# Kernel optimization log

Measured on AMD Instinct MI355X. Metric: run time of the kernel, lower is better.

## Reference

```python
import jax, jax.numpy as jnp
import numpy as np

NUM_NODES = 100000
NUM_REL = 500
D = 400          # entity_out_dim[0] * nheads_GAT[0] = 200 * 2
C = 50           # conv_out_channels
B = 16384        # batch of triples


def setup_inputs() -> dict:
    key = jax.random.key(0)
    k = jax.random.split(key, 7)
    entity_emb = jax.random.normal(k[0], (NUM_NODES, D), jnp.float32)
    relation_emb = jax.random.normal(k[1], (NUM_REL, D), jnp.float32)
    # Conv2d(1, C, (1, 3)) weight: [C, 1, 1, 3]; xavier-ish scale
    conv_w = jax.random.normal(k[2], (C, 1, 1, 3), jnp.float32) * 0.5
    conv_b = jnp.zeros((C,), jnp.float32)
    # Linear(D*C, 1)
    fc_w = jax.random.normal(k[3], (1, D * C), jnp.float32) * 0.01
    fc_b = jnp.zeros((1,), jnp.float32)
    heads = jax.random.randint(k[4], (B,), 0, NUM_NODES)
    rels = jax.random.randint(k[5], (B,), 0, NUM_REL)
    tails = jax.random.randint(k[6], (B,), 0, NUM_NODES)
    batch_inputs = jnp.stack([heads, rels, tails], axis=1)  # [B, 3]
    return {
        "entity_emb": entity_emb,
        "relation_emb": relation_emb,
        "conv_w": conv_w,
        "conv_b": conv_b,
        "fc_w": fc_w,
        "fc_b": fc_b,
        "batch_inputs": batch_inputs,
    }


def reference(entity_emb, relation_emb, conv_w, conv_b, fc_w, fc_b, batch_inputs):
    # Gather (h, r, t) rows: irregular access into large tables
    h = entity_emb[batch_inputs[:, 0]]    # [B, D]
    r = relation_emb[batch_inputs[:, 1]]  # [B, D]
    t = entity_emb[batch_inputs[:, 2]]    # [B, D]
    # torch: cat -> [B, 3, D], transpose -> [B, D, 3], unsqueeze -> [B, 1, D, 3]
    x = jnp.stack([h, r, t], axis=-1)     # [B, D, 3]
    # Conv2d(1, C, (1, 3)): kernel spans full width -> per-channel dot over 3
    w = conv_w[:, 0, 0, :]                # [C, 3]
    out = jnp.einsum("bdk,ck->bcd", x, w) + conv_b[None, :, None]  # [B, C, D]
    out = jax.nn.relu(out)                # dropout is identity in eval mode
    # squeeze(-1).view(B, -1): channel-major flatten -> [B, C*D]
    flat = out.reshape(out.shape[0], -1)
    return flat @ fc_w.T + fc_b           # [B, 1]
```

## Files before the change

### kernel.cpp

```cpp
#include <hip/hip_runtime.h>


typedef _Float16 h2 __attribute__((ext_vector_type(2)));
typedef _Float16 h8 __attribute__((ext_vector_type(8)));

constexpr int D    = 400;
constexpr int CP   = 25;
constexpr int DPAD = 404;

static __device__ __forceinline__ float dot2acc(h2 a, h2 b, float c) {
#if __has_builtin(__builtin_amdgcn_fdot2)
    return __builtin_amdgcn_fdot2(a, b, c, false);
#else
    h2 p = a * b; return c + (float)p[0] + (float)p[1];
#endif
}
static __device__ __forceinline__ h2 dup(float v) {
    _Float16 x = (_Float16)v; h2 r; r[0] = x; r[1] = x; return r;
}

__global__ __attribute__((amdgpu_flat_work_group_size(512, 512), amdgpu_waves_per_eu(2, 4)))
void grcnet_pk16g(
    const float* __restrict__ entity_emb,
    const float* __restrict__ relation_emb,
    const float* __restrict__ conv_w,
    const float* __restrict__ conv_b,
    const float* __restrict__ fc_w,
    const float* __restrict__ fc_b,
    const int*   __restrict__ batch_inputs,
    float* __restrict__ out,
    int nB)
{
    __shared__ h2    fc_lds[CP + 1][DPAD];
    __shared__ h2    conv_lds[CP + 1][4];
    __shared__ float partials[2][2][4][4];

    const int tid  = threadIdx.x;
    const int lane = tid & 63;
    const int wv   = tid >> 6;
    const int grp  = wv >> 1;
    const int hc   = wv & 1;
    const int bq   = blockIdx.x * 32;
    if (bq >= nB) return;

    const float *p0h, *p0r, *p0t, *p1h, *p1r, *p1t;
    const float *p2h, *p2r, *p2t, *p3h, *p3r, *p3t;

    #define SETPTRS(B0)                                                           \
    {                                                                             \
        const int bbase = __builtin_amdgcn_readfirstlane((B0) + 4 * grp);         \
        const int* bi = batch_inputs + 3 * bbase;                                 \
        p0h = entity_emb   + (size_t)bi[0]  * D + lane;                           \
        p0r = relation_emb + (size_t)bi[1]  * D + lane;                           \
        p0t = entity_emb   + (size_t)bi[2]  * D + lane;                           \
        p1h = entity_emb   + (size_t)bi[3]  * D + lane;                           \
        p1r = relation_emb + (size_t)bi[4]  * D + lane;                           \
        p1t = entity_emb   + (size_t)bi[5]  * D + lane;                           \
        p2h = entity_emb   + (size_t)bi[6]  * D + lane;                           \
        p2r = relation_emb + (size_t)bi[7]  * D + lane;                           \
        p2t = entity_emb   + (size_t)bi[8]  * D + lane;                           \
        p3h = entity_emb   + (size_t)bi[9]  * D + lane;                           \
        p3r = relation_emb + (size_t)bi[10] * D + lane;                           \
        p3t = entity_emb   + (size_t)bi[11] * D + lane;                           \
    }

    #define LOADI(S, IDX)                                                         \
        f##S##_0h = p0h[IDX]; f##S##_0r = p0r[IDX]; f##S##_0t = p0t[IDX];         \
        f##S##_1h = p1h[IDX]; f##S##_1r = p1r[IDX]; f##S##_1t = p1t[IDX];         \
        f##S##_2h = p2h[IDX]; f##S##_2r = p2r[IDX]; f##S##_2t = p2t[IDX];         \
        f##S##_3h = p3h[IDX]; f##S##_3r = p3r[IDX]; f##S##_3t = p3t[IDX];

    float fA_0h, fA_0r, fA_0t, fA_1h, fA_1r, fA_1t;
    float fA_2h, fA_2r, fA_2t, fA_3h, fA_3r, fA_3t;
    float fB_0h, fB_0r, fB_0t, fB_1h, fB_1r, fB_1t;
    float fB_2h, fB_2r, fB_2t, fB_3h, fB_3r, fB_3t;

    SETPTRS(bq)
    LOADI(A, 0)
    LOADI(B, 64)

    for (int k = tid; k < CP * 100; k += 512) {
        const int cp = k / 100;
        const int dq = k - cp * 100;
        const float4 A  = *(const float4*)(fc_w + (2*cp)     * D + 4*dq);
        const float4 Bv = *(const float4*)(fc_w + (2*cp + 1) * D + 4*dq);
        h8 g;
        g[0]=(_Float16)A.x; g[1]=(_Float16)Bv.x;
        g[2]=(_Float16)A.y; g[3]=(_Float16)Bv.y;
        g[4]=(_Float16)A.z; g[5]=(_Float16)Bv.z;
        g[6]=(_Float16)A.w; g[7]=(_Float16)Bv.w;
        *(h8*)&fc_lds[cp][4*dq] = g;
    }
    {
        h2 z; z[0] = (_Float16)0; z[1] = (_Float16)0;
        if (tid < CP * 4) fc_lds[tid >> 2][D + (tid & 3)] = z;
        if (tid >= 64 && tid < 64 + DPAD) fc_lds[CP][tid - 64] = z;
    }
    if (tid < CP + 1) {
        const int src = (tid == CP) ? (CP - 1) : tid;
        const int c0 = 2 * src;
        h2 wa, wb, wc, cb;
        wa[0]=(_Float16)conv_w[3*c0+0]; wa[1]=(_Float16)conv_w[3*c0+3];
        wb[0]=(_Float16)conv_w[3*c0+1]; wb[1]=(_Float16)conv_w[3*c0+4];
        wc[0]=(_Float16)conv_w[3*c0+2]; wc[1]=(_Float16)conv_w[3*c0+5];
        cb[0]=(_Float16)conv_b[c0];     cb[1]=(_Float16)conv_b[c0+1];
        conv_lds[tid][0]=wa; conv_lds[tid][1]=wb;
        conv_lds[tid][2]=wc; conv_lds[tid][3]=cb;
    }
    __syncthreads();

    const int C0 = 13 * hc;
    constexpr int NC = 13;
    h2 cwa[NC], cwb[NC], cwc[NC], ccb[NC];
    #pragma unroll
    for (int j = 0; j < NC; ++j) {
        cwa[j] = conv_lds[C0+j][0]; cwb[j] = conv_lds[C0+j][1];
        cwc[j] = conv_lds[C0+j][2]; ccb[j] = conv_lds[C0+j][3];
    }

    const int  d6 = lane + 384;
    const bool a6 = (d6 < D);
    const int  i6 = a6 ? 384 : -lane;
    const h2* fcb  = &fc_lds[0][0] + C0 * DPAD + lane;
    const h2* fcb6 = &fc_lds[0][0] + C0 * DPAD + (a6 ? d6 : D);

    const h2 zero2 = (h2)(_Float16)0;

    #define COMPUTE(S, FB, FIDX0)                                                 \
    {                                                                             \
        const h2 H0 = dup(f##S##_0h), R0 = dup(f##S##_0r), T0 = dup(f##S##_0t);   \
        const h2 H1 = dup(f##S##_1h), R1 = dup(f##S##_1r), T1 = dup(f##S##_1t);   \
        const h2 H2 = dup(f##S##_2h), R2 = dup(f##S##_2r), T2 = dup(f##S##_2t);   \
        const h2 H3 = dup(f##S##_3h), R3 = dup(f##S##_3r), T3 = dup(f##S##_3t);   \
        _Pragma("unroll")                                                         \
        for (int j = 0; j < NC; ++j) {                                            \
            const h2 f2 = (FB)[(FIDX0) + j * DPAD];               \
            h2 s0 = H0*cwa[j] + (R0*cwb[j] + (T0*cwc[j] + ccb[j]));               \
            h2 s1 = H1*cwa[j] + (R1*cwb[j] + (T1*cwc[j] + ccb[j]));               \
            h2 s2 = H2*cwa[j] + (R2*cwb[j] + (T2*cwc[j] + ccb[j]));               \
            h2 s3 = H3*cwa[j] + (R3*cwb[j] + (T3*cwc[j] + ccb[j]));               \
            s0 = __builtin_elementwise_max(s0, zero2);                            \
            s1 = __builtin_elementwise_max(s1, zero2);                            \
            s2 = __builtin_elementwise_max(s2, zero2);                            \
            s3 = __builtin_elementwise_max(s3, zero2);                            \
            acc0 = dot2acc(s0, f2, acc0);                                         \
            acc1 = dot2acc(s1, f2, acc1);                                         \
            acc2 = dot2acc(s2, f2, acc2);                                         \
            acc3 = dot2acc(s3, f2, acc3);                                         \
        }                                                                         \
    }

    #pragma unroll 1
    for (int g = 0; g < 2; ++g) {
        const int b0 = bq + 16 * g;
        if (b0 >= nB) break;
        if (g) {
            SETPTRS(b0)
            LOADI(A, 0)
            LOADI(B, 64)
        }
        float acc0 = 0.f, acc1 = 0.f, acc2 = 0.f, acc3 = 0.f;

        LOADI(A, 128)
        (void)0;
        acc0 = 0.f; acc1 = 0.f; acc2 = 0.f; acc3 = 0.f;
        if (g) { LOADI(A, 0) LOADI(B, 64) }
        else   { LOADI(A, 0) LOADI(B, 64) }

        COMPUTE(A, fcb, 0*64)   LOADI(A, 128)
        COMPUTE(B, fcb, 1*64)   LOADI(B, 192)
        COMPUTE(A, fcb, 2*64)   LOADI(A, 256)
        COMPUTE(B, fcb, 3*64)   LOADI(B, 320)
        COMPUTE(A, fcb, 4*64)   LOADI(A, i6)
        COMPUTE(B, fcb, 5*64)
        COMPUTE(A, fcb6, 0)

        #pragma unroll
        for (int off = 32; off > 0; off >>= 1) {
            acc0 += __shfl_xor(acc0, off);
            acc1 += __shfl_xor(acc1, off);
            acc2 += __shfl_xor(acc2, off);
            acc3 += __shfl_xor(acc3, off);
        }
        if (lane == 0) {
            partials[g][hc][grp][0] = acc0; partials[g][hc][grp][1] = acc1;
            partials[g][hc][grp][2] = acc2; partials[g][hc][grp][3] = acc3;
        }
    }
    #undef COMPUTE
    #undef LOADI
    #undef SETPTRS

    __syncthreads();

    if (tid < 32) {
        const int g = tid >> 4, idx = tid & 15;
        const int gr = idx >> 2, j = idx & 3;
        const int b = bq + 16 * g + 4 * gr + j;
        if (b < nB)
            out[b] = partials[g][0][gr][j] + partials[g][1][gr][j] + fc_b[0];
    }
}

extern "C" void kernel_launch(void* const* d_in, const int* in_sizes, int n_in,
                              void* d_out, int out_size, void* d_ws, size_t ws_size,
                              hipStream_t stream) {
    const float* entity_emb   = (const float*)d_in[0];
    const float* relation_emb = (const float*)d_in[1];
    const float* conv_w       = (const float*)d_in[2];
    const float* conv_b       = (const float*)d_in[3];
    const float* fc_w         = (const float*)d_in[4];
    const float* fc_b         = (const float*)d_in[5];
    const int*   batch_inputs = (const int*)d_in[6];
    float* out = (float*)d_out;

    const int nB = in_sizes[6] / 3;
    const int blocks = (nB + 31) / 32;
    grcnet_pk16g<<<blocks, 512, 0, stream>>>(
        entity_emb, relation_emb, conv_w, conv_b, fc_w, fc_b, batch_inputs, out, nB);
}
```

Baseline: 44.87 us.

## Move conv weights to scalar registers and raise occupancy target

```diff
diff --git a/kernel.cpp b/kernel.cpp
--- a/kernel.cpp
+++ b/kernel.cpp
@@ -18,9 +18,12 @@
 static __device__ __forceinline__ h2 dup(float v) {
     _Float16 x = (_Float16)v; h2 r; r[0] = x; r[1] = x; return r;
 }
-
-__global__ __attribute__((amdgpu_flat_work_group_size(512, 512), amdgpu_waves_per_eu(2, 4)))
-void grcnet_pk16g(
+static __device__ __forceinline__ h2 s2h(unsigned u) {
+    return __builtin_bit_cast(h2, u);
+}
+
+__global__ __attribute__((amdgpu_flat_work_group_size(512, 512), amdgpu_waves_per_eu(6, 8)))
+void grcnet_pk16i(
     const float* __restrict__ entity_emb,
     const float* __restrict__ relation_emb,
     const float* __restrict__ conv_w,
@@ -75,9 +78,7 @@
     float fB_0h, fB_0r, fB_0t, fB_1h, fB_1r, fB_1t;
     float fB_2h, fB_2r, fB_2t, fB_3h, fB_3r, fB_3t;
 
-    SETPTRS(bq)
-    LOADI(A, 0)
-    LOADI(B, 64)
+    const h2 zero2 = (h2)(_Float16)0;
 
     for (int k = tid; k < CP * 100; k += 512) {
         const int cp = k / 100;
@@ -111,11 +112,14 @@
 
     const int C0 = 13 * hc;
     constexpr int NC = 13;
-    h2 cwa[NC], cwb[NC], cwc[NC], ccb[NC];
+
+    unsigned cwa_u[NC], cwb_u[NC], cwc_u[NC], ccb_u[NC];
     #pragma unroll
     for (int j = 0; j < NC; ++j) {
-        cwa[j] = conv_lds[C0+j][0]; cwb[j] = conv_lds[C0+j][1];
-        cwc[j] = conv_lds[C0+j][2]; ccb[j] = conv_lds[C0+j][3];
+        cwa_u[j] = __builtin_amdgcn_readfirstlane(__builtin_bit_cast(unsigned, conv_lds[C0+j][0]));
+        cwb_u[j] = __builtin_amdgcn_readfirstlane(__builtin_bit_cast(unsigned, conv_lds[C0+j][1]));
+        cwc_u[j] = __builtin_amdgcn_readfirstlane(__builtin_bit_cast(unsigned, conv_lds[C0+j][2]));
+        ccb_u[j] = __builtin_amdgcn_readfirstlane(__builtin_bit_cast(unsigned, conv_lds[C0+j][3]));
     }
 
     const int  d6 = lane + 384;
@@ -124,21 +128,21 @@
     const h2* fcb  = &fc_lds[0][0] + C0 * DPAD + lane;
     const h2* fcb6 = &fc_lds[0][0] + C0 * DPAD + (a6 ? d6 : D);
 
-    const h2 zero2 = (h2)(_Float16)0;
-
     #define COMPUTE(S, FB, FIDX0)                                                 \
     {                                                                             \
-        const h2 H0 = dup(f##S##_0h), R0 = dup(f##S##_0r), T0 = dup(f##S##_0t);   \
-        const h2 H1 = dup(f##S##_1h), R1 = dup(f##S##_1r), T1 = dup(f##S##_1t);   \
-        const h2 H2 = dup(f##S##_2h), R2 = dup(f##S##_2r), T2 = dup(f##S##_2t);   \
-        const h2 H3 = dup(f##S##_3h), R3 = dup(f##S##_3r), T3 = dup(f##S##_3t);   \
+        const h2 H0=dup(f##S##_0h), R0=dup(f##S##_0r), T0=dup(f##S##_0t);         \
+        const h2 H1=dup(f##S##_1h), R1=dup(f##S##_1r), T1=dup(f##S##_1t);         \
+        const h2 H2=dup(f##S##_2h), R2=dup(f##S##_2r), T2=dup(f##S##_2t);         \
+        const h2 H3=dup(f##S##_3h), R3=dup(f##S##_3r), T3=dup(f##S##_3t);         \
         _Pragma("unroll")                                                         \
         for (int j = 0; j < NC; ++j) {                                            \
+            const h2 wa = s2h(cwa_u[j]), wb = s2h(cwb_u[j]);                      \
+            const h2 wc = s2h(cwc_u[j]), cb = s2h(ccb_u[j]);                      \
             const h2 f2 = (FB)[(FIDX0) + j * DPAD];               \
-            h2 s0 = H0*cwa[j] + (R0*cwb[j] + (T0*cwc[j] + ccb[j]));               \
-            h2 s1 = H1*cwa[j] + (R1*cwb[j] + (T1*cwc[j] + ccb[j]));               \
-            h2 s2 = H2*cwa[j] + (R2*cwb[j] + (T2*cwc[j] + ccb[j]));               \
-            h2 s3 = H3*cwa[j] + (R3*cwb[j] + (T3*cwc[j] + ccb[j]));               \
+            h2 s0 = H0*wa + (R0*wb + (T0*wc + cb));                               \
+            h2 s1 = H1*wa + (R1*wb + (T1*wc + cb));                               \
+            h2 s2 = H2*wa + (R2*wb + (T2*wc + cb));                               \
+            h2 s3 = H3*wa + (R3*wb + (T3*wc + cb));                               \
             s0 = __builtin_elementwise_max(s0, zero2);                            \
             s1 = __builtin_elementwise_max(s1, zero2);                            \
             s2 = __builtin_elementwise_max(s2, zero2);                            \
@@ -153,19 +157,10 @@
     #pragma unroll 1
     for (int g = 0; g < 2; ++g) {
         const int b0 = bq + 16 * g;
-        if (b0 >= nB) break;
-        if (g) {
-            SETPTRS(b0)
-            LOADI(A, 0)
-            LOADI(B, 64)
-        }
+        SETPTRS(b0)
+        LOADI(A, 0)
+        LOADI(B, 64)
         float acc0 = 0.f, acc1 = 0.f, acc2 = 0.f, acc3 = 0.f;
-
-        LOADI(A, 128)
-        (void)0;
-        acc0 = 0.f; acc1 = 0.f; acc2 = 0.f; acc3 = 0.f;
-        if (g) { LOADI(A, 0) LOADI(B, 64) }
-        else   { LOADI(A, 0) LOADI(B, 64) }
 
         COMPUTE(A, fcb, 0*64)   LOADI(A, 128)
         COMPUTE(B, fcb, 1*64)   LOADI(B, 192)
@@ -216,6 +211,6 @@
 
     const int nB = in_sizes[6] / 3;
     const int blocks = (nB + 31) / 32;
-    grcnet_pk16g<<<blocks, 512, 0, stream>>>(
+    grcnet_pk16i<<<blocks, 512, 0, stream>>>(
         entity_emb, relation_emb, conv_w, conv_b, fc_w, fc_b, batch_inputs, out, nB);
 }
```

New measurement: 104.5 us. +132.8%, slower.
